# Performance work log

Hardware: AMD Instinct MI355X
Metric: run time of the kernel (lower is better)

The kernel has to match this reference:

```python
import jax, jax.numpy as jnp
import numpy as np

D_MODEL = 768
NUM_HEADS = 12
HEAD_DIM = D_MODEL // NUM_HEADS


def setup_inputs() -> dict:
    key = jax.random.key(0)
    ks = jax.random.split(key, 9)
    B, S = 2, 2048
    s = 1.0 / np.sqrt(D_MODEL)
    x = jax.random.normal(ks[0], (B, S, D_MODEL), dtype=jnp.float32)
    Wq = jax.random.normal(ks[1], (D_MODEL, D_MODEL), dtype=jnp.float32) * s
    Wk = jax.random.normal(ks[2], (D_MODEL, D_MODEL), dtype=jnp.float32) * s
    Wv = jax.random.normal(ks[3], (D_MODEL, D_MODEL), dtype=jnp.float32) * s
    Wo = jax.random.normal(ks[4], (D_MODEL, D_MODEL), dtype=jnp.float32) * s
    bq = jax.random.normal(ks[5], (D_MODEL,), dtype=jnp.float32) * 0.01
    bk = jax.random.normal(ks[6], (D_MODEL,), dtype=jnp.float32) * 0.01
    bv = jax.random.normal(ks[7], (D_MODEL,), dtype=jnp.float32) * 0.01
    bo = jax.random.normal(ks[8], (D_MODEL,), dtype=jnp.float32) * 0.01
    return {"x": x, "Wq": Wq, "bq": bq, "Wk": Wk, "bk": bk,
            "Wv": Wv, "bv": bv, "Wo": Wo, "bo": bo}


def reference(x, Wq, bq, Wk, bk, Wv, bv, Wo, bo):
    B, S, _ = x.shape
    # projections; reshape to [B, H, S, Dh]
    def split_heads(t):
        return t.reshape(B, S, NUM_HEADS, HEAD_DIM).transpose(0, 2, 1, 3)
    q = split_heads(x @ Wq + bq)
    k = split_heads(x @ Wk + bk)
    v = split_heads(x @ Wv + bv)
    scale = 1.0 / np.sqrt(HEAD_DIM)
    scores = jnp.einsum("bhqd,bhkd->bhqk", q, k) * scale  # [B,H,S,S]
    attn = jax.nn.softmax(scores, axis=-1)
    # dropout p=0.0 (eval) -> identity
    ctx = jnp.einsum("bhqk,bhkd->bhqd", attn, v)
    ctx = ctx.transpose(0, 2, 1, 3).reshape(B, S, D_MODEL)
    return ctx @ Wo + bo
```

## Files before the change

### kernel.cpp

```cpp
#include <hip/hip_runtime.h>
#include <hip/hip_bf16.h>
#include <hip/hip_fp16.h>

#define D_MODEL 768
#define NHEADS  12
#define HD      64
#define BATCH   2
#define SEQ     2048
#define NTOK    (BATCH*SEQ)
#define NX      ((size_t)NTOK * D_MODEL)
#define NW      ((size_t)D_MODEL * D_MODEL)
#define NBH     (BATCH*NHEADS)
#define SC_LOG2 0.18033688f

typedef __attribute__((ext_vector_type(8))) short    short8;
typedef __attribute__((ext_vector_type(8))) _Float16 half8;
typedef __attribute__((ext_vector_type(2))) __fp16   fp16x2;
typedef __attribute__((ext_vector_type(4))) float    f32x4;

__device__ __forceinline__ float bf2f(short s) {
    union { unsigned u; float f; } c;
    c.u = ((unsigned)(unsigned short)s) << 16;
    return c.f;
}
__device__ __forceinline__ short f2bf(float f) {
    __hip_bfloat16 h = __float2bfloat16(f);
    return *(short*)&h;
}

#ifdef __has_builtin
#if __has_builtin(__builtin_amdgcn_global_load_lds)
#define HAS_GLD 1
#endif
#if __has_builtin(__builtin_amdgcn_exp2f)
#define EXP2(x) __builtin_amdgcn_exp2f(x)
#else
#define EXP2(x) exp2f(x)
#endif
#if __has_builtin(__builtin_amdgcn_cvt_pkrtz)
#define HAS_PKRTZ 1
#endif
#else
#define EXP2(x) exp2f(x)
#endif
#ifdef HAS_GLD
#define GLD16(gp, lp) __builtin_amdgcn_global_load_lds( \
    (const __attribute__((address_space(1))) void*)(gp), \
    (__attribute__((address_space(3))) void*)(lp), 16, 0, 0)
#endif

#ifdef HAS_PKRTZ
#define PKF16(a, b) __builtin_amdgcn_cvt_pkrtz((a), (b))
#else
#define PKF16(a, b) ((fp16x2){ (__fp16)(a), (__fp16)(b) })
#endif

__global__ __launch_bounds__(256) void fused_conv(
        const void* __restrict__ xin,
        const void* __restrict__ w0, const void* __restrict__ w1,
        const void* __restrict__ w2, const void* __restrict__ w3,
        const void* __restrict__ b0, const void* __restrict__ b1,
        const void* __restrict__ b2, const void* __restrict__ b3,
        short* __restrict__ xc, short* __restrict__ wt,
        short* __restrict__ bc, int* __restrict__ flag)
{
    __shared__ int red[256];
    __shared__ float T[64][65];
    const int tid = threadIdx.x;
    const int F = blockIdx.x;

    {
        const short* xs = (const short*)xin;
        int maxe = 0;
#pragma unroll
        for (int u = 0; u < 16; ++u) {
            int e = ((unsigned short)xs[tid * 16 + u] >> 7) & 0xFF;
            maxe = max(maxe, e);
        }
        red[tid] = maxe;
        __syncthreads();
        for (int s = 128; s > 0; s >>= 1) {
            if (tid < s) red[tid] = max(red[tid], red[tid + s]);
            __syncthreads();
        }
    }
    const bool isf = (red[0] > 140);

    if (F < 3072) {
        const int i = F * 256 + tid;
        if (isf) {
            float4 f = ((const float4*)xin)[i];
            short4 o = { f2bf(f.x), f2bf(f.y), f2bf(f.z), f2bf(f.w) };
            ((short4*)xc)[i] = o;
        } else {
            ((short4*)xc)[i] = ((const short4*)xin)[i];
        }
    } else if (F < 3648) {
        const int G = F - 3072;
        const int z = G / 144, rr = G % 144;
        const int k0 = (rr % 12) * 64, n0 = (rr / 12) * 64;
        const void* src = (z == 0) ? w0 : (z == 1) ? w1 : (z == 2) ? w2 : w3;
        const float sc = (z == 0) ? SC_LOG2 : 1.0f;
        const int la = tid & 15, lb = tid >> 4;
#pragma unroll
        for (int u = 0; u < 4; ++u) {
            const int kr = (lb & 3) + 4 * u + 16 * (lb >> 2);
            if (isf) {
                float4 f = *(const float4*)((const float*)src + (size_t)(k0 + kr) * D_MODEL + n0 + la * 4);
                T[kr][la*4+0] = f.x; T[kr][la*4+1] = f.y; T[kr][la*4+2] = f.z; T[kr][la*4+3] = f.w;
            } else {
                short4 s = *(const short4*)((const short*)src + (size_t)(k0 + kr) * D_MODEL + n0 + la * 4);
                T[kr][la*4+0] = bf2f(s.x); T[kr][la*4+1] = bf2f(s.y);
                T[kr][la*4+2] = bf2f(s.z); T[kr][la*4+3] = bf2f(s.w);
            }
        }
        __syncthreads();
#pragma unroll
        for (int u = 0; u < 4; ++u) {
            const int nr = (lb & 3) + 4 * u + 16 * (lb >> 2);
            short4 o = { f2bf(T[la*4+0][nr] * sc), f2bf(T[la*4+1][nr] * sc),
                         f2bf(T[la*4+2][nr] * sc), f2bf(T[la*4+3][nr] * sc) };
            *(short4*)(wt + (size_t)z * NW + (size_t)(n0 + nr) * D_MODEL + k0 + la * 4) = o;
        }
    } else {
        if (tid == 0) *flag = isf ? 1 : 0;
        const void* srcs[4] = { b0, b1, b2, b3 };
        for (int z = 0; z < 4; ++z) {
            const float sc = (z == 0) ? SC_LOG2 : 1.0f;
            for (int i = tid; i < D_MODEL; i += 256) {
                float v = isf ? ((const float*)srcs[z])[i] : bf2f(((const short*)srcs[z])[i]);
                bc[z * D_MODEL + i] = f2bf(v * sc);
            }
        }
    }
}

__global__ __launch_bounds__(512) void qkv_gemm(const short* __restrict__ X,
                                                const short* __restrict__ Wt,
                                                const short* __restrict__ bias,
                                                short* __restrict__ qb,
                                                short* __restrict__ kb,
                                                _Float16* __restrict__ Vt)
{
    __shared__ __align__(16) char shbuf[32768];
    short* Als = (short*)shbuf;
    short* Bls = (short*)(shbuf + 16384);
    _Float16* T = (_Float16*)shbuf;

    const int tid = threadIdx.x;
    const int wave = tid >> 6, lane = tid & 63;
    const int quad = lane >> 4, l16 = lane & 15;
    const int wm = wave & 3, wn = wave >> 2;
    const int m0 = blockIdx.x * 128;
    const int ng = blockIdx.y * 128;

    f32x4 acc[2][4];
#pragma unroll
    for (int nt = 0; nt < 4; ++nt) {
        const float bv = bf2f(bias[ng + wn*64 + nt*16 + l16]);
#pragma unroll
        for (int mt = 0; mt < 2; ++mt) acc[mt][nt] = (f32x4){bv, bv, bv, bv};
    }

    const int row = tid >> 2, ch = (tid & 3) * 8;
#ifdef HAS_GLD
#define QSTAGE(buf, k0) do { \
        GLD16(X  + (size_t)(m0 + row) * D_MODEL + (k0) + ch, &Als[(buf)*4096 + tid*8]); \
        GLD16(Wt + (size_t)(ng + row) * D_MODEL + (k0) + ch, &Bls[(buf)*4096 + tid*8]); \
    } while (0)
#else
#define QSTAGE(buf, k0) do { \
        short8 r0 = *(const short8*)(X  + (size_t)(m0 + row) * D_MODEL + (k0) + ch); \
        short8 r1 = *(const short8*)(Wt + (size_t)(ng + row) * D_MODEL + (k0) + ch); \
        *(short8*)&Als[(buf)*4096 + tid*8] = r0; \
        *(short8*)&Bls[(buf)*4096 + tid*8] = r1; \
    } while (0)
#endif

    QSTAGE(0, 0);
    __syncthreads();

    for (int ks = 0; ks < 24; ++ks) {
        const int cur = ks & 1;
        if (ks + 1 < 24) QSTAGE(cur ^ 1, (ks + 1) * 32);

        short8 a[2], b[4];
#pragma unroll
        for (int mt = 0; mt < 2; ++mt)
            a[mt] = *(const short8*)&Als[cur*4096 + (wm*32 + mt*16 + l16) * 32 + quad*8];
#pragma unroll
        for (int nt = 0; nt < 4; ++nt)
            b[nt] = *(const short8*)&Bls[cur*4096 + (wn*64 + nt*16 + l16) * 32 + quad*8];
#pragma unroll
        for (int mt = 0; mt < 2; ++mt)
#pragma unroll
        for (int nt = 0; nt < 4; ++nt)
            acc[mt][nt] = __builtin_amdgcn_mfma_f32_16x16x32_bf16(a[mt], b[nt], acc[mt][nt], 0, 0, 0);

        __syncthreads();
    }
#undef QSTAGE

    const int seg = blockIdx.y / 6;
    if (seg == 0) {
#pragma unroll
        for (int mt = 0; mt < 2; ++mt)
#pragma unroll
        for (int nt = 0; nt < 4; ++nt) {
            const int n = ng + wn*64 + nt*16 + l16;
#pragma unroll
            for (int r = 0; r < 4; ++r) {
                const int m = m0 + wm*32 + mt*16 + quad*4 + r;
                qb[(size_t)m * D_MODEL + n] = f2bf(acc[mt][nt][r]);
            }
        }
    } else if (seg == 1) {
        const int nl = ng - 768;
#pragma unroll
        for (int mt = 0; mt < 2; ++mt)
#pragma unroll
        for (int nt = 0; nt < 4; ++nt) {
            const int n = nl + wn*64 + nt*16 + l16;
            const int h = n >> 6, dh = n & 63;
            const int chunk = dh >> 3, dof = dh & 7;
#pragma unroll
            for (int r = 0; r < 4; ++r) {
                const int m = m0 + wm*32 + mt*16 + quad*4 + r;
                const int b2 = m >> 11, tok = m & (SEQ - 1);
                kb[((size_t)(b2*NHEADS + h)*32 + (tok >> 6))*4096
                   + chunk*512 + (tok & 63)*8 + dof] = f2bf(acc[mt][nt][r]);
            }
        }
    } else {
        const int batch = m0 >> 11, tokb0 = m0 & (SEQ - 1);
#pragma unroll
        for (int p = 0; p < 2; ++p) {
            if ((wm >> 1) == p) {
#pragma unroll
                for (int nt = 0; nt < 4; ++nt) {
                    const int dim_l = wn*64 + nt*16 + l16;
#pragma unroll
                    for (int mt = 0; mt < 2; ++mt) {
                        const int tok_l = (wm & 1)*32 + mt*16 + quad*4;
                        union { _Float16 h4[4]; int2 v; } u;
#pragma unroll
                        for (int r = 0; r < 4; ++r) u.h4[r] = (_Float16)acc[mt][nt][r];
                        *(int2*)&T[dim_l * 72 + tok_l] = u.v;
                    }
                }
            }
            __syncthreads();
#pragma unroll
            for (int u = 0; u < 2; ++u) {
                const int slot = tid + u * 512;
                const int drow = slot & 127, chk = slot >> 7;
                int4 val = *(const int4*)&T[drow * 72 + chk * 8];
                const int dim_g = ng - 1536 + drow;
                const int h = dim_g >> 6, dl = dim_g & 63;
                *(int4*)(Vt + ((size_t)((batch*NHEADS + h)*32) + (tokb0 >> 6) + p)*4096
                            + chk*512 + dl*8) = val;
            }
            if (p == 0) __syncthreads();
        }
    }
}

__global__ __launch_bounds__(256) void out_gemm(const _Float16* __restrict__ Op,
                                                const float* __restrict__ mlp,
                                                const short* __restrict__ Wt,
                                                const short* __restrict__ bias,
                                                void* __restrict__ outv,
                                                const int* __restrict__ flag)
{
    __shared__ short Als[2][2048];
    __shared__ short Bls[2][2048];

    const int tid = threadIdx.x;
    const int wave = tid >> 6, lane = tid & 63;
    const int quad = lane >> 4, l16 = lane & 15;
    const int m0 = blockIdx.x * 64;
    const int n0 = blockIdx.y * 64;

    f32x4 acc[4];
#pragma unroll
    for (int nt = 0; nt < 4; ++nt) {
        const float bv = bf2f(bias[n0 + nt*16 + l16]);
        acc[nt] = (f32x4){bv, bv, bv, bv};
    }

    const int row = tid >> 2, ch = (tid & 3) * 8;
    const int m = m0 + row;
    const int bhb = (m >> 11) * NHEADS;
    const int qq = m & (SEQ - 1);
    const _Float16* Op2 = Op + (size_t)(NBH * SEQ) * HD;

#define XLOAD(ks) do { \
        const int cc = (ks) * 32 + ch; \
        const int h = cc >> 6, d = cc & 63; \
        const size_t r1 = (size_t)(bhb + h) * SEQ + qq; \
        const float2 ml1 = *(const float2*)&mlp[r1 * 2]; \
        const float2 ml2 = *(const float2*)&mlp[((size_t)(NBH * SEQ) + r1) * 2]; \
        p1 = *(const half8*)&Op[r1 * HD + d]; \
        p2 = *(const half8*)&Op2[r1 * HD + d]; \
        const float M_ = fmaxf(ml1.x, ml2.x); \
        const float w1 = EXP2(ml1.x - M_) * ml1.y; \
        const float w2 = EXP2(ml2.x - M_) * ml2.y; \
        const float s_ = 1.0f / (w1 + w2); \
        f1 = w1 * s_; f2 = w2 * s_; \
    } while (0)

#define XSTORE(buf) do { \
        short8 xb; \
        _Pragma("unroll") \
        for (int j = 0; j < 8; ++j) \
            xb[j] = f2bf(f1 * (float)p1[j] + f2 * (float)p2[j]); \
        *(short8*)&Als[buf][tid*8] = xb; \
    } while (0)

#ifdef HAS_GLD
#define BSTAGE(buf, k0) \
        GLD16(Wt + (size_t)(n0 + row) * D_MODEL + (k0) + ch, &Bls[buf][tid*8])
#else
#define BSTAGE(buf, k0) do { \
        short8 r1_ = *(const short8*)(Wt + (size_t)(n0 + row) * D_MODEL + (k0) + ch); \
        *(short8*)&Bls[buf][tid*8] = r1_; } while (0)
#endif

    half8 p1, p2; float f1, f2;
    XLOAD(0); XSTORE(0);
    BSTAGE(0, 0);
    __syncthreads();

    for (int ks = 0; ks < 24; ++ks) {
        const int cur = ks & 1;
        if (ks + 1 < 24) {
            XLOAD(ks + 1);
            BSTAGE(cur ^ 1, (ks + 1) * 32);
        }

        short8 a = *(const short8*)&Als[cur][(wave*16 + l16) * 32 + quad*8];
#pragma unroll
        for (int nt = 0; nt < 4; ++nt) {
            short8 b = *(const short8*)&Bls[cur][(nt*16 + l16) * 32 + quad*8];
            acc[nt] = __builtin_amdgcn_mfma_f32_16x16x32_bf16(a, b, acc[nt], 0, 0, 0);
        }

        if (ks + 1 < 24) XSTORE(cur ^ 1);
        __syncthreads();
    }
#undef XLOAD
#undef XSTORE
#undef BSTAGE

    const bool outf32 = (*flag != 0);
#pragma unroll
    for (int nt = 0; nt < 4; ++nt) {
        const int n = n0 + nt*16 + l16;
#pragma unroll
        for (int r = 0; r < 4; ++r) {
            const int mm = m0 + wave*16 + quad*4 + r;
            const size_t idx = (size_t)mm * D_MODEL + n;
            if (outf32) ((float*)outv)[idx] = acc[nt][r];
            else        ((short*)outv)[idx] = f2bf(acc[nt][r]);
        }
    }
}

__global__ __launch_bounds__(256, 3) void attn_mfma(const short* __restrict__ q,
                                                    const short* __restrict__ k,
                                                    const _Float16* __restrict__ Vt,
                                                    _Float16* __restrict__ Op,
                                                    float* __restrict__ mlp)
{
    __shared__ __align__(16) short    Kls[2][4096];
    __shared__ __align__(16) _Float16 Vls[2][4096];
    __shared__ __align__(16) _Float16 Pls[4][2048];

    const int tid  = threadIdx.x;
    const int wave = tid >> 6, lane = tid & 63;
    const int quad = lane >> 4, l16 = lane & 15;

    const int F = blockIdx.x;
    const int xcd = F & 7, slot = F >> 3;
    const int bh = xcd * 3 + (slot >> 5);
    const int rem = slot & 31;
    const int q0 = (rem >> 1) * 128;
    const int sp = rem & 1;
    const int b = bh / NHEADS, h = bh % NHEADS;
    const size_t bS = (size_t)b * SEQ;

    short8 qf[2][2];
#pragma unroll
    for (int col = 0; col < 2; ++col)
#pragma unroll
    for (int k0h = 0; k0h < 2; ++k0h)
        qf[col][k0h] = *(const short8*)(q + (bS + q0 + wave*32 + col*16 + l16) * D_MODEL
                                          + h*HD + k0h*32 + quad*8);

    half8 ones;
#pragma unroll
    for (int j = 0; j < 8; ++j) ones[j] = (_Float16)1.0f;

    const short*    kbase = k  + ((size_t)bh*32 + sp*16) * 4096;
    const _Float16* vbase = Vt + ((size_t)bh*32 + sp*16) * 4096;

#ifdef HAS_GLD
#define STAGE_K(buf, j0) do { \
        GLD16(kbase + (size_t)(j0)*64 + tid*8,       &Kls[buf][tid*8]); \
        GLD16(kbase + (size_t)(j0)*64 + (tid+256)*8, &Kls[buf][(tid+256)*8]); \
    } while (0)
#define STAGE_V(buf, j0) do { \
        GLD16(vbase + (size_t)(j0)*64 + tid*8,       &Vls[buf][tid*8]); \
        GLD16(vbase + (size_t)(j0)*64 + (tid+256)*8, &Vls[buf][(tid+256)*8]); \
    } while (0)
#else
#define STAGE_K(buf, j0) do { \
        short8 a_ = *(const short8*)(kbase + (size_t)(j0)*64 + tid*8); \
        short8 b_ = *(const short8*)(kbase + (size_t)(j0)*64 + (tid+256)*8); \
        *(short8*)&Kls[buf][tid*8] = a_;  *(short8*)&Kls[buf][(tid+256)*8] = b_; \
    } while (0)
#define STAGE_V(buf, j0) do { \
        half8 c_ = *(const half8*)(vbase + (size_t)(j0)*64 + tid*8); \
        half8 d_ = *(const half8*)(vbase + (size_t)(j0)*64 + (tid+256)*8); \
        *(half8*)&Vls[buf][tid*8] = c_;  *(half8*)&Vls[buf][(tid+256)*8] = d_; \
    } while (0)
#endif

    float m_ = -1e30f;
    f32x4 laccA = (f32x4){0.f,0.f,0.f,0.f}, laccB = (f32x4){0.f,0.f,0.f,0.f};
    f32x4 o[4][2];
#pragma unroll
    for (int t = 0; t < 4; ++t) { o[t][0] = (f32x4){0.f,0.f,0.f,0.f}; o[t][1] = (f32x4){0.f,0.f,0.f,0.f}; }

#define NT (SEQ / 2 / 64)

#define QK(S, KB) do { \
    _Pragma("unroll") \
    for (int t = 0; t < 4; ++t) { S[t][0] = (f32x4){0.f,0.f,0.f,0.f}; S[t][1] = (f32x4){0.f,0.f,0.f,0.f}; } \
    _Pragma("unroll") \
    for (int k0h = 0; k0h < 2; ++k0h) \
    _Pragma("unroll") \
    for (int t = 0; t < 4; ++t) { \
        short8 kf = *(const short8*)&Kls[KB][(k0h*4 + quad)*512 + (t*16 + l16)*8]; \
        S[t][0] = __builtin_amdgcn_mfma_f32_16x16x32_bf16(kf, qf[0][k0h], S[t][0], 0, 0, 0); \
        S[t][1] = __builtin_amdgcn_mfma_f32_16x16x32_bf16(kf, qf[1][k0h], S[t][1], 0, 0, 0); \
    } \
} while (0)

#define PV(VB) do { \
    _Pragma("unroll") \
    for (int k0h = 0; k0h < 2; ++k0h) { \
        half8 pf0 = *(half8*)&Pls[wave][(k0h*4 + quad)*128 + l16*8]; \
        half8 pf1 = *(half8*)&Pls[wave][1024 + (k0h*4 + quad)*128 + l16*8]; \
        laccA = __builtin_amdgcn_mfma_f32_16x16x32_f16(ones, pf0, laccA, 0, 0, 0); \
        laccB = __builtin_amdgcn_mfma_f32_16x16x32_f16(ones, pf1, laccB, 0, 0, 0); \
        _Pragma("unroll") \
        for (int t = 0; t < 4; ++t) { \
            half8 vf = *(const half8*)&Vls[VB][(k0h*4 + quad)*512 + (t*16 + l16)*8]; \
            o[t][0] = __builtin_amdgcn_mfma_f32_16x16x32_f16(vf, pf0, o[t][0], 0, 0, 0); \
            o[t][1] = __builtin_amdgcn_mfma_f32_16x16x32_f16(vf, pf1, o[t][1], 0, 0, 0); \
        } \
    } \
} while (0)

#define SOFTMAX(S) do { \
    float mx = S[0][0][0]; \
    _Pragma("unroll") \
    for (int t = 0; t < 4; ++t) \
    _Pragma("unroll") \
    for (int c = 0; c < 2; ++c) \
    _Pragma("unroll") \
    for (int r = 0; r < 4; ++r) mx = fmaxf(mx, S[t][c][r]); \
    if (__any(mx > m_ + 8.f)) { \
        _Pragma("unroll") \
        for (int d = 1; d < 64; d <<= 1) mx = fmaxf(mx, __shfl_xor(mx, d)); \
        const float mn = fmaxf(m_, mx); \
        const float al = EXP2(m_ - mn); \
        _Pragma("unroll") \
        for (int t = 0; t < 4; ++t) \
        _Pragma("unroll") \
        for (int c = 0; c < 2; ++c) { \
            o[t][c][0] *= al; o[t][c][1] *= al; o[t][c][2] *= al; o[t][c][3] *= al; \
        } \
        laccA[0] *= al; laccB[0] *= al; \
        m_ = mn; \
    } \
    _Pragma("unroll") \
    for (int t = 0; t < 4; ++t) \
    _Pragma("unroll") \
    for (int c = 0; c < 2; ++c) { \
        union { fp16x2 h2[2]; int2 v; } u4; \
        u4.h2[0] = PKF16(EXP2(S[t][c][0] - m_), EXP2(S[t][c][1] - m_)); \
        u4.h2[1] = PKF16(EXP2(S[t][c][2] - m_), EXP2(S[t][c][3] - m_)); \
        const int kc = 2*t + (quad >> 1); \
        *(int2*)&Pls[wave][c*1024 + kc*128 + l16*8 + (quad & 1)*4] = u4.v; \
    } \
} while (0)

#define BODY(JT) do { \
    if ((JT) + 2 < NT) STAGE_K(((JT) + 2) & 1, ((JT) + 2) * 64); \
    if ((JT) + 1 < NT) STAGE_V(((JT) + 1) & 1, ((JT) + 1) * 64); \
    f32x4 s_[4][2]; \
    __builtin_amdgcn_s_setprio(1); \
    if ((JT) + 1 < NT) QK(s_, ((JT) + 1) & 1); \
    PV((JT) & 1); \
    __builtin_amdgcn_s_setprio(0); \
    if ((JT) + 1 < NT) SOFTMAX(s_); \
    __syncthreads(); \
} while (0)

    STAGE_K(0, 0); STAGE_V(0, 0);
    __syncthreads();
    STAGE_K(1, 64);
    {
        f32x4 s_[4][2];
        QK(s_, 0);
        SOFTMAX(s_);
    }
    __syncthreads();

    for (int jt = 0; jt < NT; ++jt) BODY(jt);

#pragma unroll
    for (int col = 0; col < 2; ++col) {
        const f32x4 la = col ? laccB : laccA;
        const float inv = 1.0f / la[0];
        const int myq = q0 + wave*32 + col*16 + l16;
        const size_t prow = ((size_t)sp * (NBH * SEQ) + (size_t)bh * SEQ + myq);
        _Float16* orow = Op + prow * HD;
#pragma unroll
        for (int t = 0; t < 4; ++t) {
            union { _Float16 h4[4]; int2 v; } u4;
#pragma unroll
            for (int r = 0; r < 4; ++r) u4.h4[r] = (_Float16)(o[t][col][r] * inv);
            *(int2*)(orow + t*16 + quad*4) = u4.v;
        }
        if (quad == 0) {
            float2 mlv; mlv.x = m_; mlv.y = la[0];
            *(float2*)&mlp[prow * 2] = mlv;
        }
    }
#undef BODY
#undef SOFTMAX
#undef PV
#undef QK
#undef NT
#undef STAGE_K
#undef STAGE_V
}

extern "C" void kernel_launch(void* const* d_in, const int* in_sizes, int n_in,
                              void* d_out, int out_size, void* d_ws, size_t ws_size,
                              hipStream_t stream)
{
    int* flag = (int*)d_ws;
    short* xc = (short*)((char*)d_ws + 64);
    short* Wt = xc + NX;
    short* bc = Wt + 4 * NW;
    short* qb = bc + 4 * D_MODEL;
    short* kb = qb + NX;
    _Float16* Vt = (_Float16*)(kb + NX);
    _Float16* Op = (_Float16*)(Vt + NX);
    float* mlp = (float*)(Op + (size_t)2 * NBH * SEQ * HD);

    fused_conv<<<3649, 256, 0, stream>>>(d_in[0],
                                         d_in[1], d_in[3], d_in[5], d_in[7],
                                         d_in[2], d_in[4], d_in[6], d_in[8],
                                         xc, Wt, bc, flag);

    qkv_gemm<<<dim3(NTOK/128, 2304/128), 512, 0, stream>>>(xc, Wt, bc, qb, kb, Vt);

    attn_mfma<<<768, 256, 0, stream>>>(qb, kb, Vt, Op, mlp);

    out_gemm<<<dim3(NTOK/64, D_MODEL/64), 256, 0, stream>>>(Op, mlp, Wt + 3*NW, bc + 3*D_MODEL, d_out, flag);
}
```

Baseline: 166.2 us.

## Fuse x fp32-to-bf16 conversion into QKV GEMM and swizzle block order

Removes the separate x conversion pass from the prep kernel: the QKV GEMM now reads fp32 x directly, converts to bf16 in registers and stores it to LDS, skipping a full write and re-read of x. Both GEMMs remap block indices with a modulo-8 swizzle, intended to spread tiles across XCDs or improve L2 locality. The output GEMM computes the softmax merge weights once per head instead of every k-step. The fp32 path gives up the async global-to-LDS load for the A operand, which may reduce overlap in the QKV GEMM main loop.

```diff
diff --git a/kernel.cpp b/kernel.cpp
--- a/kernel.cpp
+++ b/kernel.cpp
@@ -61,8 +61,7 @@
         const void* __restrict__ w2, const void* __restrict__ w3,
         const void* __restrict__ b0, const void* __restrict__ b1,
         const void* __restrict__ b2, const void* __restrict__ b3,
-        short* __restrict__ xc, short* __restrict__ wt,
-        short* __restrict__ bc, int* __restrict__ flag)
+        short* __restrict__ wt, short* __restrict__ bc, int* __restrict__ flag)
 {
     __shared__ int red[256];
     __shared__ float T[64][65];
@@ -86,18 +85,8 @@
     }
     const bool isf = (red[0] > 140);
 
-    if (F < 3072) {
-        const int i = F * 256 + tid;
-        if (isf) {
-            float4 f = ((const float4*)xin)[i];
-            short4 o = { f2bf(f.x), f2bf(f.y), f2bf(f.z), f2bf(f.w) };
-            ((short4*)xc)[i] = o;
-        } else {
-            ((short4*)xc)[i] = ((const short4*)xin)[i];
-        }
-    } else if (F < 3648) {
-        const int G = F - 3072;
-        const int z = G / 144, rr = G % 144;
+    if (F < 576) {
+        const int z = F / 144, rr = F % 144;
         const int k0 = (rr % 12) * 64, n0 = (rr / 12) * 64;
         const void* src = (z == 0) ? w0 : (z == 1) ? w1 : (z == 2) ? w2 : w3;
         const float sc = (z == 0) ? SC_LOG2 : 1.0f;
@@ -135,9 +124,10 @@
     }
 }
 
-__global__ __launch_bounds__(512) void qkv_gemm(const short* __restrict__ X,
+__global__ __launch_bounds__(512) void qkv_gemm(const void* __restrict__ X,
                                                 const short* __restrict__ Wt,
                                                 const short* __restrict__ bias,
+                                                const int* __restrict__ flag,
                                                 short* __restrict__ qb,
                                                 short* __restrict__ kb,
                                                 _Float16* __restrict__ Vt)
@@ -151,8 +141,14 @@
     const int wave = tid >> 6, lane = tid & 63;
     const int quad = lane >> 4, l16 = lane & 15;
     const int wm = wave & 3, wn = wave >> 2;
-    const int m0 = blockIdx.x * 128;
-    const int ng = blockIdx.y * 128;
+
+    const int lin = blockIdx.x + blockIdx.y * gridDim.x;
+    const int wg  = (lin & 7) * 72 + (lin >> 3);
+    const int bx  = wg & 31, by = wg >> 5;
+    const int m0 = bx * 128;
+    const int ng = by * 128;
+
+    const bool isf = (*flag != 0);
 
     f32x4 acc[2][4];
 #pragma unroll
@@ -163,19 +159,33 @@
     }
 
     const int row = tid >> 2, ch = (tid & 3) * 8;
+#define ASTAGE(buf, k0) do { \
+        if (isf) { \
+            const float* xp = (const float*)X + (size_t)(m0 + row) * D_MODEL + (k0) + ch; \
+            float4 fa = *(const float4*)xp; \
+            float4 fb = *(const float4*)(xp + 4); \
+            short8 xb; \
+            xb[0]=f2bf(fa.x); xb[1]=f2bf(fa.y); xb[2]=f2bf(fa.z); xb[3]=f2bf(fa.w); \
+            xb[4]=f2bf(fb.x); xb[5]=f2bf(fb.y); xb[6]=f2bf(fb.z); xb[7]=f2bf(fb.w); \
+            *(short8*)&Als[(buf)*4096 + tid*8] = xb; \
+        } else { \
+            BF16_A(buf, k0); \
+        } \
+    } while (0)
 #ifdef HAS_GLD
-#define QSTAGE(buf, k0) do { \
-        GLD16(X  + (size_t)(m0 + row) * D_MODEL + (k0) + ch, &Als[(buf)*4096 + tid*8]); \
-        GLD16(Wt + (size_t)(ng + row) * D_MODEL + (k0) + ch, &Bls[(buf)*4096 + tid*8]); \
-    } while (0)
+#define BF16_A(buf, k0) \
+        GLD16((const short*)X + (size_t)(m0 + row) * D_MODEL + (k0) + ch, &Als[(buf)*4096 + tid*8])
+#define BSTAGE(buf, k0) \
+        GLD16(Wt + (size_t)(ng + row) * D_MODEL + (k0) + ch, &Bls[(buf)*4096 + tid*8])
 #else
-#define QSTAGE(buf, k0) do { \
-        short8 r0 = *(const short8*)(X  + (size_t)(m0 + row) * D_MODEL + (k0) + ch); \
+#define BF16_A(buf, k0) do { \
+        short8 r0 = *(const short8*)((const short*)X + (size_t)(m0 + row) * D_MODEL + (k0) + ch); \
+        *(short8*)&Als[(buf)*4096 + tid*8] = r0; } while (0)
+#define BSTAGE(buf, k0) do { \
         short8 r1 = *(const short8*)(Wt + (size_t)(ng + row) * D_MODEL + (k0) + ch); \
-        *(short8*)&Als[(buf)*4096 + tid*8] = r0; \
-        *(short8*)&Bls[(buf)*4096 + tid*8] = r1; \
-    } while (0)
-#endif
+        *(short8*)&Bls[(buf)*4096 + tid*8] = r1; } while (0)
+#endif
+#define QSTAGE(buf, k0) do { ASTAGE(buf, k0); BSTAGE(buf, k0); } while (0)
 
     QSTAGE(0, 0);
     __syncthreads();
@@ -200,8 +210,11 @@
         __syncthreads();
     }
 #undef QSTAGE
-
-    const int seg = blockIdx.y / 6;
+#undef ASTAGE
+#undef BF16_A
+#undef BSTAGE
+
+    const int seg = by / 6;
     if (seg == 0) {
 #pragma unroll
         for (int mt = 0; mt < 2; ++mt)
@@ -278,8 +291,11 @@
     const int tid = threadIdx.x;
     const int wave = tid >> 6, lane = tid & 63;
     const int quad = lane >> 4, l16 = lane & 15;
-    const int m0 = blockIdx.x * 64;
-    const int n0 = blockIdx.y * 64;
+
+    const int lin = blockIdx.x + blockIdx.y * gridDim.x;
+    const int wg  = (lin & 7) * 96 + (lin >> 3);
+    const int m0 = (wg & 63) * 64;
+    const int n0 = (wg >> 6) * 64;
 
     f32x4 acc[4];
 #pragma unroll
@@ -294,19 +310,22 @@
     const int qq = m & (SEQ - 1);
     const _Float16* Op2 = Op + (size_t)(NBH * SEQ) * HD;
 
-#define XLOAD(ks) do { \
-        const int cc = (ks) * 32 + ch; \
-        const int h = cc >> 6, d = cc & 63; \
-        const size_t r1 = (size_t)(bhb + h) * SEQ + qq; \
+#define MLOAD(h) do { \
+        const size_t r1 = (size_t)(bhb + (h)) * SEQ + qq; \
         const float2 ml1 = *(const float2*)&mlp[r1 * 2]; \
         const float2 ml2 = *(const float2*)&mlp[((size_t)(NBH * SEQ) + r1) * 2]; \
-        p1 = *(const half8*)&Op[r1 * HD + d]; \
-        p2 = *(const half8*)&Op2[r1 * HD + d]; \
         const float M_ = fmaxf(ml1.x, ml2.x); \
         const float w1 = EXP2(ml1.x - M_) * ml1.y; \
         const float w2 = EXP2(ml2.x - M_) * ml2.y; \
         const float s_ = 1.0f / (w1 + w2); \
         f1 = w1 * s_; f2 = w2 * s_; \
+    } while (0)
+
+#define PLOAD(ks) do { \
+        const int d = ((ks) & 1) * 32 + ch; \
+        const size_t r1 = (size_t)(bhb + ((ks) >> 1)) * SEQ + qq; \
+        p1 = *(const half8*)&Op[r1 * HD + d]; \
+        p2 = *(const half8*)&Op2[r1 * HD + d]; \
     } while (0)
 
 #define XSTORE(buf) do { \
@@ -327,14 +346,15 @@
 #endif
 
     half8 p1, p2; float f1, f2;
-    XLOAD(0); XSTORE(0);
+    MLOAD(0); PLOAD(0); XSTORE(0);
     BSTAGE(0, 0);
     __syncthreads();
 
     for (int ks = 0; ks < 24; ++ks) {
         const int cur = ks & 1;
         if (ks + 1 < 24) {
-            XLOAD(ks + 1);
+            if (((ks + 1) & 1) == 0) MLOAD((ks + 1) >> 1);
+            PLOAD(ks + 1);
             BSTAGE(cur ^ 1, (ks + 1) * 32);
         }
 
@@ -348,7 +368,8 @@
         if (ks + 1 < 24) XSTORE(cur ^ 1);
         __syncthreads();
     }
-#undef XLOAD
+#undef MLOAD
+#undef PLOAD
 #undef XSTORE
 #undef BSTAGE
 
@@ -554,8 +575,7 @@
                               hipStream_t stream)
 {
     int* flag = (int*)d_ws;
-    short* xc = (short*)((char*)d_ws + 64);
-    short* Wt = xc + NX;
+    short* Wt = (short*)((char*)d_ws + 64);
     short* bc = Wt + 4 * NW;
     short* qb = bc + 4 * D_MODEL;
     short* kb = qb + NX;
@@ -563,14 +583,14 @@
     _Float16* Op = (_Float16*)(Vt + NX);
     float* mlp = (float*)(Op + (size_t)2 * NBH * SEQ * HD);
 
-    fused_conv<<<3649, 256, 0, stream>>>(d_in[0],
-                                         d_in[1], d_in[3], d_in[5], d_in[7],
-                                         d_in[2], d_in[4], d_in[6], d_in[8],
-                                         xc, Wt, bc, flag);
-
-    qkv_gemm<<<dim3(NTOK/128, 2304/128), 512, 0, stream>>>(xc, Wt, bc, qb, kb, Vt);
+    fused_conv<<<577, 256, 0, stream>>>(d_in[0],
+                                        d_in[1], d_in[3], d_in[5], d_in[7],
+                                        d_in[2], d_in[4], d_in[6], d_in[8],
+                                        Wt, bc, flag);
+
+    qkv_gemm<<<dim3(32, 18), 512, 0, stream>>>(d_in[0], Wt, bc, flag, qb, kb, Vt);
 
     attn_mfma<<<768, 256, 0, stream>>>(qb, kb, Vt, Op, mlp);
 
-    out_gemm<<<dim3(NTOK/64, D_MODEL/64), 256, 0, stream>>>(Op, mlp, Wt + 3*NW, bc + 3*D_MODEL, d_out, flag);
-}
+    out_gemm<<<dim3(64, 12), 256, 0, stream>>>(Op, mlp, Wt + 3*NW, bc + 3*D_MODEL, d_out, flag);
+}
```

After: 192.1 us. +15.6%, slower.
